# Optimization experiments

Hardware: AMD Instinct MI355X
Metric: run time of the kernel (lower is better)

Reference implementation:

```python
import jax, jax.numpy as jnp
import numpy as np

N = 50000
E = 1600000
EPS = 1e-16


def transformer_conv(x, src, dst, ea, Wq, bq, Wk, bk, Wv, bv, We, Ws, bs):
    # PyG TransformerConv, heads=1, concat=True, root_weight=True
    C = Wq.shape[1]
    q = x @ Wq + bq                      # [N, C]
    k = x @ Wk + bk                      # [N, C]
    v = x @ Wv + bv                      # [N, C]
    e = ea @ We                          # [E, C]
    k_e = k[src] + e                     # per-edge key
    v_e = v[src] + e                     # per-edge value
    score = (q[dst] * k_e).sum(-1) / jnp.sqrt(jnp.asarray(C, x.dtype))  # [E]
    # segment softmax over incoming edges of each dst node
    m = jax.ops.segment_max(score, dst, num_segments=N)
    ex = jnp.exp(score - m[dst])
    denom = jax.ops.segment_sum(ex, dst, num_segments=N)
    alpha = ex / (denom[dst] + EPS)
    out = jax.ops.segment_sum(alpha[:, None] * v_e, dst, num_segments=N)
    return out + x @ Ws + bs             # skip connection


def gcn_conv(x, src, dst, W, b):
    # PyG GCNConv: self-loops + symmetric deg^-1/2 normalization
    n_idx = jnp.arange(N)
    src2 = jnp.concatenate([src, n_idx])
    dst2 = jnp.concatenate([dst, n_idx])
    deg = jax.ops.segment_sum(jnp.ones(E + N, x.dtype), dst2, num_segments=N)
    dinv = jnp.where(deg > 0, jax.lax.rsqrt(deg), 0.0)
    norm = dinv[src2] * dinv[dst2]       # [E+N]
    h = x @ W                            # [N, out]
    out = jax.ops.segment_sum(norm[:, None] * h[src2], dst2, num_segments=N)
    return out + b


def setup_inputs() -> dict:
    key = jax.random.key(0)
    ks = jax.random.split(key, 32)
    d = {}
    d['x'] = jax.random.normal(ks[0], (N, 128), jnp.float32)
    d['edge_index'] = jax.random.randint(ks[1], (2, E), 0, N, jnp.int64)
    d['edge_attr'] = jax.random.normal(ks[2], (E, 16), jnp.float32)
    shapes = dict(
        Wq1=(128, 96), bq1=(96,), Wk1=(128, 96), bk1=(96,), Wv1=(128, 96), bv1=(96,),
        We1=(16, 96), Ws1=(128, 96), bs1=(96,),
        Wq2=(96, 64), bq2=(64,), Wk2=(96, 64), bk2=(64,), Wv2=(96, 64), bv2=(64,),
        We2=(16, 64), Ws2=(96, 64), bs2=(64,),
        Wmu=(64, 32), bmu=(32,), Wls=(64, 32), bls=(32,))
    for i, (name, shp) in enumerate(shapes.items()):
        scale = 1.0 / np.sqrt(shp[0]) if len(shp) == 2 else 0.02
        d[name] = jax.random.normal(ks[3 + i], shp, jnp.float32) * scale
    return d


def reference(x, edge_index, edge_attr,
              Wq1, bq1, Wk1, bk1, Wv1, bv1, We1, Ws1, bs1,
              Wq2, bq2, Wk2, bk2, Wv2, bv2, We2, Ws2, bs2,
              Wmu, bmu, Wls, bls):
    src, dst = edge_index[0], edge_index[1]
    h = jax.nn.relu(transformer_conv(x, src, dst, edge_attr,
                                     Wq1, bq1, Wk1, bk1, Wv1, bv1, We1, Ws1, bs1))
    h = jax.nn.relu(transformer_conv(h, src, dst, edge_attr,
                                     Wq2, bq2, Wk2, bk2, Wv2, bv2, We2, Ws2, bs2))
    mu = gcn_conv(h, src, dst, Wmu, bmu)
    logstd = gcn_conv(h, src, dst, Wls, bls)
    return mu, logstd
```

## Files before the change

kernel.cpp:

```cpp
#include <hip/hip_runtime.h>
#include <math.h>


#define TPB 256
typedef unsigned int uint32;
typedef unsigned short ushort16;
typedef __attribute__((ext_vector_type(4))) float f32x4;
typedef __attribute__((ext_vector_type(8))) short bf16x8;

__device__ __forceinline__ uint32 f2bf(float f) {
    uint32 u = __float_as_uint(f);
    return (u + 0x7fffu + ((u >> 16) & 1u)) >> 16;
}
__device__ __forceinline__ float bf2f(uint32 b) { return __uint_as_float(b << 16); }

__global__ void hist_kernel(const int* __restrict__ dst, int* __restrict__ deg, int E) {
    int i = blockIdx.x * TPB + threadIdx.x;
    if (i < E) atomicAdd(&deg[dst[i]], 1);
}

__global__ __launch_bounds__(1024) void scan1_kernel(const int* __restrict__ deg,
                                                     int* __restrict__ rowp,
                                                     int* __restrict__ bsum, int n) {
    __shared__ int wsum[16];
    __shared__ int woff[16];
    int tid = threadIdx.x;
    int i = blockIdx.x * 1024 + tid;
    int lane = tid & 63, w = tid >> 6;
    int x = (i < n) ? deg[i] : 0;
    int v = x;
#pragma unroll
    for (int off = 1; off < 64; off <<= 1) {
        int t = __shfl_up(v, off, 64);
        if (lane >= off) v += t;
    }
    if (lane == 63) wsum[w] = v;
    __syncthreads();
    if (tid < 64) {
        int s = (tid < 16) ? wsum[tid] : 0;
#pragma unroll
        for (int off = 1; off < 16; off <<= 1) {
            int t = __shfl_up(s, off, 64);
            if (lane >= off) s += t;
        }
        if (tid < 16) woff[tid] = s;
    }
    __syncthreads();
    int incl = v + (w ? woff[w - 1] : 0);
    if (i < n) rowp[i] = incl;
    if (tid == 1023) bsum[blockIdx.x] = incl;
}

__global__ void scan2_kernel(const int* __restrict__ bsum, int* __restrict__ boff, int nb) {
    int tid = threadIdx.x;
    int x = (tid < nb) ? bsum[tid] : 0;
    int v = x;
#pragma unroll
    for (int off = 1; off < 64; off <<= 1) {
        int t = __shfl_up(v, off, 64);
        if (tid >= off) v += t;
    }
    if (tid < nb) boff[tid] = v - x;
}

__global__ __launch_bounds__(1024) void scan3_kernel(const int* __restrict__ deg,
                                                     const int* __restrict__ boff,
                                                     int* __restrict__ rowp,
                                                     int* __restrict__ cursor,
                                                     float* __restrict__ dinv,
                                                     int n, int E) {
    int i = blockIdx.x * 1024 + threadIdx.x;
    if (i < n) {
        int d = deg[i];
        int excl = rowp[i] - d + boff[blockIdx.x];
        rowp[i] = excl;
        cursor[i] = excl;
        dinv[i] = 1.0f / sqrtf((float)(d + 1));
    }
    if (i == 0) rowp[n] = E;
}

__global__ void scatter_kernel(const int* __restrict__ src, const int* __restrict__ dst,
                               const float* __restrict__ EA,
                               int* __restrict__ cursor,
                               int* __restrict__ psrc, ushort16* __restrict__ EAb, int E) {
    int i = blockIdx.x * TPB + threadIdx.x;
    if (i >= E) return;
    int pos = atomicAdd(&cursor[dst[i]], 1);
    psrc[pos] = src[i];
    const float4* e4 = (const float4*)(EA + (size_t)i * 16);
    float4 a = e4[0], b = e4[1], c = e4[2], d = e4[3];
    uint32* o = (uint32*)(EAb + (size_t)pos * 16);
    o[0] = f2bf(a.x) | (f2bf(a.y) << 16);
    o[1] = f2bf(a.z) | (f2bf(a.w) << 16);
    o[2] = f2bf(b.x) | (f2bf(b.y) << 16);
    o[3] = f2bf(b.z) | (f2bf(b.w) << 16);
    o[4] = f2bf(c.x) | (f2bf(c.y) << 16);
    o[5] = f2bf(c.z) | (f2bf(c.w) << 16);
    o[6] = f2bf(d.x) | (f2bf(d.y) << 16);
    o[7] = f2bf(d.z) | (f2bf(d.w) << 16);
}

__global__ void pack_kernel(
    const float* Wq1, const float* Wk1, const float* Wv1, const float* Ws1,
    const float* bq1, const float* bk1, const float* bv1, const float* bs1,
    const float* We1,
    const float* Wq2, const float* Wk2, const float* Wv2, const float* Ws2,
    const float* bq2, const float* bk2, const float* bv2, const float* bs2,
    const float* We2,
    const float* Wmu, const float* bmu, const float* Wls, const float* bls,
    unsigned short* Wc1t, float* bc1, unsigned short* Wc2t, float* bc2,
    float* Wc3, float* bc3) {
    const float s1 = 0.1020620726159658f;
    const float s2 = 0.125f;
    int i = blockIdx.x * TPB + threadIdx.x;
    const int R0 = 448 * 128, R1 = R0 + 320 * 96, R2 = R1 + 64 * 64;
    const int R3 = R2 + 448, R4 = R3 + 320, R5 = R4 + 64;
    if (i < R0) {
        int c = i / 128, kk = i % 128;
        float v = 0.f;
        if (c < 96) v = Wq1[kk * 96 + c] * s1;
        else if (c < 112) {
            int t = c - 96; float a = 0.f;
            for (int u = 0; u < 96; ++u) a += Wq1[kk * 96 + u] * We1[t * 96 + u];
            v = a * s1;
        } else if (c < 304) {
            int tt = c - 112;
            v = (tt & 1) ? Wv1[kk * 96 + (tt >> 1)] : Wk1[kk * 96 + (tt >> 1)];
        } else if (c < 400) v = Ws1[kk * 96 + (c - 304)];
        Wc1t[i] = (unsigned short)f2bf(v);
    } else if (i < R1) {
        int j = i - R0;
        int c = j / 96, kk = j % 96;
        float v = 0.f;
        if (c < 64) v = Wq2[kk * 64 + c] * s2;
        else if (c < 80) {
            int t = c - 64; float a = 0.f;
            for (int u = 0; u < 64; ++u) a += Wq2[kk * 64 + u] * We2[t * 64 + u];
            v = a * s2;
        } else if (c < 208) {
            int tt = c - 80;
            v = (tt & 1) ? Wv2[kk * 64 + (tt >> 1)] : Wk2[kk * 64 + (tt >> 1)];
        } else if (c < 272) v = Ws2[kk * 64 + (c - 208)];
        Wc2t[j] = (unsigned short)f2bf(v);
    } else if (i < R2) {
        int j = i - R1;
        int k = j / 64, c = j % 64;
        Wc3[j] = (c < 32) ? Wmu[k * 32 + c] : Wls[k * 32 + (c - 32)];
    } else if (i < R3) {
        int c = i - R2;
        float v = 0.f;
        if (c < 96) v = bq1[c] * s1;
        else if (c < 112) {
            int t = c - 96; float a = 0.f;
            for (int u = 0; u < 96; ++u) a += bq1[u] * We1[t * 96 + u];
            v = a * s1;
        } else if (c < 304) {
            int tt = c - 112;
            v = (tt & 1) ? bv1[tt >> 1] : bk1[tt >> 1];
        } else if (c < 400) v = bs1[c - 304];
        bc1[c] = v;
    } else if (i < R4) {
        int c = i - R3;
        float v = 0.f;
        if (c < 64) v = bq2[c] * s2;
        else if (c < 80) {
            int t = c - 64; float a = 0.f;
            for (int u = 0; u < 64; ++u) a += bq2[u] * We2[t * 64 + u];
            v = a * s2;
        } else if (c < 208) {
            int tt = c - 80;
            v = (tt & 1) ? bv2[tt >> 1] : bk2[tt >> 1];
        } else if (c < 272) v = bs2[c - 208];
        bc2[c] = v;
    } else if (i < R5) {
        int c = i - R4;
        bc3[c] = (c < 32) ? bmu[c] : bls[c - 32];
    }
}

__global__ void xcvt_kernel(const float* __restrict__ x, unsigned short* __restrict__ xb, int n) {
    int i = blockIdx.x * TPB + threadIdx.x;
    if (i < n) xb[i] = (unsigned short)f2bf(x[i]);
}

__global__ __launch_bounds__(256) void mfma_gemm_kernel(
    const unsigned short* __restrict__ A,
    const unsigned short* __restrict__ Wt,
    const float* __restrict__ bias,
    float* __restrict__ Qs, float* __restrict__ QE,
    uint32* __restrict__ KVp, float* __restrict__ SK,
    int N, int K, int Cq) {
    __shared__ unsigned short As[64][56];
    __shared__ unsigned short Bs[64][56];
    int r0 = blockIdx.x * 64, c0 = blockIdx.y * 64;
    int tid = threadIdx.x;
    int lane = tid & 63, w = tid >> 6;
    int wm = w >> 1, wn = w & 1;
    int l15 = lane & 15, l4 = lane >> 4;
    f32x4 zero = {0.f, 0.f, 0.f, 0.f};
    f32x4 acc[2][2] = {{zero, zero}, {zero, zero}};
    int sr = tid >> 2, sk = (tid & 3) * 8;

    for (int kc = 0; kc < K; kc += 32) {
        bf16x8 av = {};
        int ar = r0 + sr;
        if (ar < N) av = *(const bf16x8*)(A + (size_t)ar * K + kc + sk);
        *(bf16x8*)&As[sr][sk] = av;
        bf16x8 bv = *(const bf16x8*)(Wt + (size_t)(c0 + sr) * K + kc + sk);
        *(bf16x8*)&Bs[sr][sk] = bv;
        __syncthreads();
        bf16x8 af0 = *(const bf16x8*)&As[32 * wm + l15][l4 * 8];
        bf16x8 af1 = *(const bf16x8*)&As[32 * wm + 16 + l15][l4 * 8];
        bf16x8 bf0 = *(const bf16x8*)&Bs[32 * wn + l15][l4 * 8];
        bf16x8 bf1 = *(const bf16x8*)&Bs[32 * wn + 16 + l15][l4 * 8];
        acc[0][0] = __builtin_amdgcn_mfma_f32_16x16x32_bf16(af0, bf0, acc[0][0], 0, 0, 0);
        acc[0][1] = __builtin_amdgcn_mfma_f32_16x16x32_bf16(af0, bf1, acc[0][1], 0, 0, 0);
        acc[1][0] = __builtin_amdgcn_mfma_f32_16x16x32_bf16(af1, bf0, acc[1][0], 0, 0, 0);
        acc[1][1] = __builtin_amdgcn_mfma_f32_16x16x32_bf16(af1, bf1, acc[1][1], 0, 0, 0);
        __syncthreads();
    }

    int qe0 = Cq, kv0 = Cq + 16, sk0 = 3 * Cq + 16, end0 = 4 * Cq + 16;
#pragma unroll
    for (int fm = 0; fm < 2; ++fm) {
#pragma unroll
        for (int fn = 0; fn < 2; ++fn) {
            int cb = c0 + 32 * wn + 16 * fn;
            int c = cb + l15;
            float bia = bias[c];
#pragma unroll
            for (int r = 0; r < 4; ++r) {
                int row = r0 + 32 * wm + 16 * fm + l4 * 4 + r;
                float v = acc[fm][fn][r] + bia;
                float pv = __shfl_xor(v, 1, 64);
                bool ok = row < N;
                if (cb < qe0) {
                    if (ok) Qs[(size_t)row * Cq + c] = v;
                } else if (cb < kv0) {
                    if (ok) QE[(size_t)row * 16 + (c - qe0)] = v;
                } else if (cb < sk0) {
                    if (ok && !(l15 & 1)) {
                        int t = c - kv0;
                        KVp[(size_t)row * Cq + (t >> 1)] = (f2bf(v) << 16) | f2bf(pv);
                    }
                } else if (cb < end0) {
                    if (ok) SK[(size_t)row * Cq + (c - sk0)] = v;
                }
            }
        }
    }
}

template <int C>
__global__ __launch_bounds__(256) void edge_attn_kernel(
    const float* __restrict__ Qs, const float* __restrict__ SK,
    const uint32* __restrict__ KVp,
    const ushort16* __restrict__ EAb, const float* __restrict__ QE,
    const int* __restrict__ rowp, const int* __restrict__ psrc,
    float* __restrict__ Hpre, float* __restrict__ AEA, int N) {
    constexpr int CPL = C / 32;
    int n = blockIdx.x * 4 + (threadIdx.x >> 6);
    if (n >= N) return;
    int lane = threadIdx.x & 63;
    int half = lane >> 5, l = lane & 31, t16 = l & 15;
    bool lo16 = (l < 16);

    float q[CPL], acc[CPL];
#pragma unroll
    for (int j = 0; j < CPL; ++j) { q[j] = Qs[(size_t)n * C + l + 32 * j]; acc[j] = 0.f; }
    float qe = lo16 ? QE[(size_t)n * 16 + t16] : 0.f;
    float d = 0.f, aea = 0.f;
    int eb = rowp[n], ee = rowp[n + 1];

    for (int base = eb + 32 * half; base < ee; base += 64) {
        int cnt = min(32, ee - base);
        int sb = (l < cnt) ? psrc[base + l] : 0;
        for (int i0 = 0; i0 < cnt; i0 += 8) {
            float dots[8], eav[8];
            uint32 kv[8][CPL];
#pragma unroll
            for (int u = 0; u < 8; ++u) {
                int i = i0 + u;
                bool ok = (i < cnt);
                int s = __shfl(sb, i & 31, 32);
                float ea = bf2f(EAb[(size_t)(base + i) * 16 + t16]);
                eav[u] = ok ? ea : 0.f;
                const uint32* kvp = KVp + (size_t)s * C;
                float dt = qe * eav[u];
#pragma unroll
                for (int j = 0; j < CPL; ++j) {
                    uint32 t = kvp[l + 32 * j];
                    kv[u][j] = t;
                    dt = fmaf(q[j], __uint_as_float(t & 0xffff0000u), dt);
                }
                dots[u] = ok ? dt : -1e30f;
            }
#pragma unroll
            for (int a = 0; a < 4; ++a) {
                float x0 = dots[2 * a], x1 = dots[2 * a + 1];
                float z = (lo16 ? x0 : x1) + __shfl_xor(lo16 ? x1 : x0, 16, 64);
                z += __shfl_xor(z, 8, 64);
                z += __shfl_xor(z, 4, 64);
                z += __shfl_xor(z, 2, 64);
                z += __shfl_xor(z, 1, 64);
                float p = __expf(z);
                float p0 = __shfl(p, 0, 32);
                float p1 = __shfl(p, 16, 32);
                d += p0 + p1;
                aea = fmaf(p0, eav[2 * a], fmaf(p1, eav[2 * a + 1], aea));
#pragma unroll
                for (int j = 0; j < CPL; ++j)
                    acc[j] = fmaf(p0, __uint_as_float(kv[2 * a][j] << 16),
                             fmaf(p1, __uint_as_float(kv[2 * a + 1][j] << 16), acc[j]));
            }
        }
    }
    d += __shfl_xor(d, 32, 64);
    aea += __shfl_xor(aea, 32, 64);
    float inv = 1.f / (d + 1e-16f);
#pragma unroll
    for (int j = 0; j < CPL; ++j) {
        float a2 = acc[j] + __shfl_xor(acc[j], 32, 64);
        if (half == 0)
            Hpre[(size_t)n * C + l + 32 * j] = a2 * inv + SK[(size_t)n * C + l + 32 * j];
    }
    if (lane < 16) AEA[(size_t)n * 16 + t16] = aea * inv;
}

template <int C>
__global__ void fixup_relu_kernel(const float* __restrict__ Hpre, const float* __restrict__ AEA,
                                  const float* __restrict__ We,
                                  unsigned short* __restrict__ H1b, int NC) {
    int idx = blockIdx.x * TPB + threadIdx.x;
    if (idx >= NC) return;
    int n = idx / C, c = idx % C;
    const float* a = AEA + (size_t)n * 16;
    float s = Hpre[idx];
#pragma unroll
    for (int t = 0; t < 16; ++t) s += a[t] * We[t * C + c];
    H1b[idx] = (unsigned short)f2bf(fmaxf(s, 0.f));
}

__global__ void fixup2_kernel(const float* __restrict__ Hpre, const float* __restrict__ AEA,
                              const float* __restrict__ We, const float* __restrict__ dinv,
                              uint32* __restrict__ H2p, int N) {
    int idx = blockIdx.x * TPB + threadIdx.x;
    if (idx >= N * 32) return;
    int n = idx >> 5, c = idx & 31;
    const float* a = AEA + (size_t)n * 16;
    float s0 = Hpre[(size_t)n * 64 + c];
    float s1 = Hpre[(size_t)n * 64 + 32 + c];
#pragma unroll
    for (int t = 0; t < 16; ++t) {
        s0 += a[t] * We[t * 64 + c];
        s1 += a[t] * We[t * 64 + 32 + c];
    }
    float dn = dinv[n];
    s0 = fmaxf(s0, 0.f) * dn;
    s1 = fmaxf(s1, 0.f) * dn;
    H2p[idx] = f2bf(s0) | (f2bf(s1) << 16);
}

__global__ __launch_bounds__(256) void gcn_agg_kernel(
    const uint32* __restrict__ H2p, const int* __restrict__ rowp,
    const int* __restrict__ psrc, const float* __restrict__ dinv,
    float* __restrict__ AGG, int N) {
    int n = blockIdx.x * 4 + (threadIdx.x >> 6);
    if (n >= N) return;
    int lane = threadIdx.x & 63, half = lane >> 5, l = lane & 31;
    float s0 = 0.f, s1 = 0.f;
    int eb = rowp[n], ee = rowp[n + 1];
    for (int base = eb + 32 * half; base < ee; base += 64) {
        int cnt = min(32, ee - base);
        int sb = (l < cnt) ? psrc[base + l] : 0;
        for (int i0 = 0; i0 < cnt; i0 += 8) {
            uint32 uu[8];
#pragma unroll
            for (int u = 0; u < 8; ++u) {
                int i = i0 + u;
                int s = __shfl(sb, i & 31, 32);
                uint32 t = H2p[(size_t)s * 32 + l];
                uu[u] = (i < cnt) ? t : 0u;
            }
#pragma unroll
            for (int u = 0; u < 8; ++u) {
                s0 += bf2f(uu[u] & 0xffffu);
                s1 += __uint_as_float(uu[u] & 0xffff0000u);
            }
        }
    }
    s0 += __shfl_xor(s0, 32, 64);
    s1 += __shfl_xor(s1, 32, 64);
    if (half == 0) {
        uint32 u = H2p[(size_t)n * 32 + l];
        float dn = dinv[n];
        AGG[(size_t)n * 64 + l]      = dn * (s0 + bf2f(u & 0xffffu));
        AGG[(size_t)n * 64 + 32 + l] = dn * (s1 + __uint_as_float(u & 0xffff0000u));
    }
}

template <int CT, bool SPLIT>
__global__ __launch_bounds__(256) void gemm_kernel(
    const float* __restrict__ A, const float* __restrict__ W,
    const float* __restrict__ bias, float* __restrict__ Out,
    float* __restrict__ Out2, int N, int K, int C) {
    constexpr int TC = CT / 16;
    __shared__ float As[32][68];
    __shared__ float Bs[32][CT + 4];
    int r0 = blockIdx.x * 64, c0 = blockIdx.y * CT;
    int t = threadIdx.x;
    int tr = t >> 4, tc = t & 15;
    float acc[4][TC];
#pragma unroll
    for (int i = 0; i < 4; ++i)
#pragma unroll
        for (int j = 0; j < TC; ++j) acc[i][j] = 0.f;

    for (int kc = 0; kc < K; kc += 32) {
        int ra = t >> 2, kq = (t & 3) * 8;
        float4 a0 = {0, 0, 0, 0}, a1 = {0, 0, 0, 0};
        int r = r0 + ra;
        if (r < N) {
            const float* ap = A + (size_t)r * K + kc + kq;
            a0 = *(const float4*)ap;
            a1 = *(const float4*)(ap + 4);
        }
        As[kq + 0][ra] = a0.x; As[kq + 1][ra] = a0.y;
        As[kq + 2][ra] = a0.z; As[kq + 3][ra] = a0.w;
        As[kq + 4][ra] = a1.x; As[kq + 5][ra] = a1.y;
        As[kq + 6][ra] = a1.z; As[kq + 7][ra] = a1.w;
        constexpr int PASSES = (32 * CT) / (256 * 8);
#pragma unroll
        for (int p = 0; p < PASSES; ++p) {
            int idx = (t + p * 256) * 8;
            int k = idx / CT, c = idx % CT;
            const float* wp = W + (size_t)(kc + k) * C + c0 + c;
            float4 b0 = *(const float4*)wp;
            float4 b1 = *(const float4*)(wp + 4);
            *(float4*)&Bs[k][c] = b0;
            *(float4*)&Bs[k][c + 4] = b1;
        }
        __syncthreads();
#pragma unroll
        for (int k = 0; k < 32; ++k) {
            float4 av = *(const float4*)&As[k][tr * 4];
            float a[4] = {av.x, av.y, av.z, av.w};
#pragma unroll
            for (int u = 0; u < TC / 4; ++u) {
                float4 bv = *(const float4*)&Bs[k][tc * TC + u * 4];
                float b[4] = {bv.x, bv.y, bv.z, bv.w};
#pragma unroll
                for (int i = 0; i < 4; ++i)
#pragma unroll
                    for (int j = 0; j < 4; ++j) acc[i][u * 4 + j] += a[i] * b[j];
            }
        }
        __syncthreads();
    }
#pragma unroll
    for (int i = 0; i < 4; ++i) {
        int r = r0 + tr * 4 + i;
        if (r >= N) continue;
#pragma unroll
        for (int j = 0; j < TC; ++j) {
            int c = c0 + tc * TC + j;
            float v = acc[i][j] + bias[c];
            if (SPLIT) {
                if (c < 32) Out[(size_t)r * 32 + c] = v;
                else        Out2[(size_t)r * 32 + c - 32] = v;
            } else {
                Out[(size_t)r * C + c] = v;
            }
        }
    }
}

extern "C" void kernel_launch(void* const* d_in, const int* in_sizes, int n_in,
                              void* d_out, int out_size, void* d_ws, size_t ws_size,
                              hipStream_t stream) {
    const float* x   = (const float*)d_in[0];
    const int*   ei  = (const int*)d_in[1];
    const float* ea  = (const float*)d_in[2];
    const float* Wq1 = (const float*)d_in[3];  const float* bq1 = (const float*)d_in[4];
    const float* Wk1 = (const float*)d_in[5];  const float* bk1 = (const float*)d_in[6];
    const float* Wv1 = (const float*)d_in[7];  const float* bv1 = (const float*)d_in[8];
    const float* We1 = (const float*)d_in[9];
    const float* Ws1 = (const float*)d_in[10]; const float* bs1 = (const float*)d_in[11];
    const float* Wq2 = (const float*)d_in[12]; const float* bq2 = (const float*)d_in[13];
    const float* Wk2 = (const float*)d_in[14]; const float* bk2 = (const float*)d_in[15];
    const float* Wv2 = (const float*)d_in[16]; const float* bv2 = (const float*)d_in[17];
    const float* We2 = (const float*)d_in[18];
    const float* Ws2 = (const float*)d_in[19]; const float* bs2 = (const float*)d_in[20];
    const float* Wmu = (const float*)d_in[21]; const float* bmu = (const float*)d_in[22];
    const float* Wls = (const float*)d_in[23]; const float* bls = (const float*)d_in[24];

    int N = in_sizes[0] / 128;
    int E = in_sizes[1] / 2;
    const int* src = ei;
    const int* dst = ei + E;

    char* ws = (char*)d_ws;
    size_t off = 0;
    auto alloc = [&](size_t bytes) -> char* {
        char* p = ws + off;
        off = (off + bytes + 255) & ~(size_t)255;
        return p;
    };
    int*      deg    = (int*)alloc((size_t)N * 4);
    int*      rowp   = (int*)alloc((size_t)(N + 1) * 4);
    int*      cursor = (int*)alloc((size_t)N * 4);
    float*    dinv   = (float*)alloc((size_t)N * 4);
    int*      bsum   = (int*)alloc(256 * 4);
    int*      boff   = (int*)alloc(256 * 4);
    int*      psrc   = (int*)alloc((size_t)E * 4);
    ushort16* EAb    = (ushort16*)alloc((size_t)E * 16 * 2);
    unsigned short* Wc1t = (unsigned short*)alloc(448 * 128 * 2);
    float*    bc1    = (float*)alloc(448 * 4);
    unsigned short* Wc2t = (unsigned short*)alloc(320 * 96 * 2);
    float*    bc2    = (float*)alloc(320 * 4);
    float*    Wc3    = (float*)alloc(64 * 64 * 4);
    float*    bc3    = (float*)alloc(64 * 4);
    unsigned short* xb = (unsigned short*)alloc((size_t)N * 128 * 2);
    float*    Qs   = (float*)alloc((size_t)N * 96 * 4);
    float*    QE   = (float*)alloc((size_t)N * 16 * 4);
    uint32*   KVp  = (uint32*)alloc((size_t)N * 96 * 4);
    float*    SKb  = (float*)alloc((size_t)N * 96 * 4);
    float*    Hpre = (float*)alloc((size_t)N * 96 * 4);
    unsigned short* H1b = (unsigned short*)alloc((size_t)N * 96 * 2);
    float*    AEA  = (float*)alloc((size_t)N * 16 * 4);
    uint32*   H2p  = (uint32*)alloc((size_t)N * 32 * 4);
    float*    AGG  = (float*)alloc((size_t)N * 64 * 4);

    hipMemsetAsync(deg, 0, (size_t)N * 4, stream);
    int ebk = (E + TPB - 1) / TPB;
    int nb1k = (N + 1023) / 1024;
    hist_kernel<<<ebk, TPB, 0, stream>>>(dst, deg, E);
    scan1_kernel<<<nb1k, 1024, 0, stream>>>(deg, rowp, bsum, N);
    scan2_kernel<<<1, 64, 0, stream>>>(bsum, boff, nb1k);
    scan3_kernel<<<nb1k, 1024, 0, stream>>>(deg, boff, rowp, cursor, dinv, N, E);
    scatter_kernel<<<ebk, TPB, 0, stream>>>(src, dst, ea, cursor, psrc, EAb, E);
    pack_kernel<<<364, TPB, 0, stream>>>(Wq1, Wk1, Wv1, Ws1, bq1, bk1, bv1, bs1, We1,
                                         Wq2, Wk2, Wv2, Ws2, bq2, bk2, bv2, bs2, We2,
                                         Wmu, bmu, Wls, bls,
                                         Wc1t, bc1, Wc2t, bc2, Wc3, bc3);
    xcvt_kernel<<<(N * 128 + TPB - 1) / TPB, TPB, 0, stream>>>(x, xb, N * 128);

    int rb = (N + 63) / 64;
    int nb4 = (N + 3) / 4;

    mfma_gemm_kernel<<<dim3(rb, 7), 256, 0, stream>>>(xb, Wc1t, bc1, Qs, QE, KVp, SKb,
                                                      N, 128, 96);
    edge_attn_kernel<96><<<nb4, 256, 0, stream>>>(Qs, SKb, KVp, EAb, QE, rowp, psrc,
                                                  Hpre, AEA, N);
    fixup_relu_kernel<96><<<(N * 96 + TPB - 1) / TPB, TPB, 0, stream>>>(Hpre, AEA, We1,
                                                                        H1b, N * 96);
    mfma_gemm_kernel<<<dim3(rb, 5), 256, 0, stream>>>(H1b, Wc2t, bc2, Qs, QE, KVp, SKb,
                                                      N, 96, 64);
    edge_attn_kernel<64><<<nb4, 256, 0, stream>>>(Qs, SKb, KVp, EAb, QE, rowp, psrc,
                                                  Hpre, AEA, N);
    fixup2_kernel<<<(N * 32 + TPB - 1) / TPB, TPB, 0, stream>>>(Hpre, AEA, We2, dinv, H2p, N);
    gcn_agg_kernel<<<nb4, 256, 0, stream>>>(H2p, rowp, psrc, dinv, AGG, N);
    gemm_kernel<64, true><<<dim3(rb, 1), 256, 0, stream>>>(AGG, Wc3, bc3, (float*)d_out,
                                                           (float*)d_out + (size_t)N * 32,
                                                           N, 64, 64);
}
```

Baseline: 532.6 us.

## Pad CSR rows to multiples of 16 with zero dummy edges to drop bounds checks

Each destination's edge list is rounded up to a multiple of 16, and the extra slots are filled with a dummy source node (index N) whose K/V and H2 rows are zeroed. The attention and GCN aggregation loops then run fixed 8-edge chunks with no shuffle-broadcast of indices and no bounds masks. The attention denominator is corrected by subtracting the pad count, since each pad edge contributes exp(0)=1. The change also folds the x-to-bf16 conversion into pack_kernel, adds nontemporal loads and stores in the edge-ordering kernels, and narrows index maths to 32 bits. The cost is up to 15 wasted edges per node (about 50% more edge traffic at an average degree of 32) and an extra padfill kernel. The unshifted sum exp(z) could also lose precision relative to the correction term.

New measurement: 623.1 us. +17.0%, slower.

```diff
diff --git a/kernel.cpp b/kernel.cpp
--- a/kernel.cpp
+++ b/kernel.cpp
@@ -4,7 +4,7 @@
 
 #define TPB 256
 typedef unsigned int uint32;
-typedef unsigned short ushort16;
+typedef unsigned short u16;
 typedef __attribute__((ext_vector_type(4))) float f32x4;
 typedef __attribute__((ext_vector_type(8))) short bf16x8;
 
@@ -16,18 +16,19 @@
 
 __global__ void hist_kernel(const int* __restrict__ dst, int* __restrict__ deg, int E) {
     int i = blockIdx.x * TPB + threadIdx.x;
-    if (i < E) atomicAdd(&deg[dst[i]], 1);
+    if (i < E) atomicAdd(&deg[__builtin_nontemporal_load(dst + i)], 1);
 }
 
 __global__ __launch_bounds__(1024) void scan1_kernel(const int* __restrict__ deg,
-                                                     int* __restrict__ rowp,
+                                                     int* __restrict__ prowp,
                                                      int* __restrict__ bsum, int n) {
     __shared__ int wsum[16];
     __shared__ int woff[16];
     int tid = threadIdx.x;
     int i = blockIdx.x * 1024 + tid;
     int lane = tid & 63, w = tid >> 6;
-    int x = (i < n) ? deg[i] : 0;
+    int dg = (i < n) ? deg[i] : 0;
+    int x = (dg + 15) & ~15;
     int v = x;
 #pragma unroll
     for (int off = 1; off < 64; off <<= 1) {
@@ -47,11 +48,12 @@
     }
     __syncthreads();
     int incl = v + (w ? woff[w - 1] : 0);
-    if (i < n) rowp[i] = incl;
+    if (i < n) prowp[i] = incl;
     if (tid == 1023) bsum[blockIdx.x] = incl;
 }
 
-__global__ void scan2_kernel(const int* __restrict__ bsum, int* __restrict__ boff, int nb) {
+__global__ void scan2_kernel(const int* __restrict__ bsum, int* __restrict__ boff,
+                             int* __restrict__ prowpN, int nb) {
     int tid = threadIdx.x;
     int x = (tid < nb) ? bsum[tid] : 0;
     int v = x;
@@ -61,44 +63,68 @@
         if (tid >= off) v += t;
     }
     if (tid < nb) boff[tid] = v - x;
+    if (tid == nb - 1) *prowpN = v;
 }
 
 __global__ __launch_bounds__(1024) void scan3_kernel(const int* __restrict__ deg,
                                                      const int* __restrict__ boff,
-                                                     int* __restrict__ rowp,
+                                                     int* __restrict__ prowp,
                                                      int* __restrict__ cursor,
-                                                     float* __restrict__ dinv,
-                                                     int n, int E) {
+                                                     float* __restrict__ dinv, int n) {
     int i = blockIdx.x * 1024 + threadIdx.x;
     if (i < n) {
-        int d = deg[i];
-        int excl = rowp[i] - d + boff[blockIdx.x];
-        rowp[i] = excl;
+        int dg = deg[i];
+        int x = (dg + 15) & ~15;
+        int excl = prowp[i] - x + boff[blockIdx.x];
+        prowp[i] = excl;
         cursor[i] = excl;
-        dinv[i] = 1.0f / sqrtf((float)(d + 1));
-    }
-    if (i == 0) rowp[n] = E;
+        dinv[i] = 1.0f / sqrtf((float)(dg + 1));
+    }
 }
 
 __global__ void scatter_kernel(const int* __restrict__ src, const int* __restrict__ dst,
                                const float* __restrict__ EA,
                                int* __restrict__ cursor,
-                               int* __restrict__ psrc, ushort16* __restrict__ EAb, int E) {
+                               int* __restrict__ psrc, u16* __restrict__ EAb, int E) {
     int i = blockIdx.x * TPB + threadIdx.x;
     if (i >= E) return;
-    int pos = atomicAdd(&cursor[dst[i]], 1);
-    psrc[pos] = src[i];
-    const float4* e4 = (const float4*)(EA + (size_t)i * 16);
-    float4 a = e4[0], b = e4[1], c = e4[2], d = e4[3];
+    int pos = atomicAdd(&cursor[__builtin_nontemporal_load(dst + i)], 1);
+    __builtin_nontemporal_store(__builtin_nontemporal_load(src + i), psrc + pos);
+    const f32x4* e4 = (const f32x4*)(EA + (size_t)i * 16);
+    f32x4 a = __builtin_nontemporal_load(e4);
+    f32x4 b = __builtin_nontemporal_load(e4 + 1);
+    f32x4 c = __builtin_nontemporal_load(e4 + 2);
+    f32x4 d = __builtin_nontemporal_load(e4 + 3);
     uint32* o = (uint32*)(EAb + (size_t)pos * 16);
-    o[0] = f2bf(a.x) | (f2bf(a.y) << 16);
-    o[1] = f2bf(a.z) | (f2bf(a.w) << 16);
-    o[2] = f2bf(b.x) | (f2bf(b.y) << 16);
-    o[3] = f2bf(b.z) | (f2bf(b.w) << 16);
-    o[4] = f2bf(c.x) | (f2bf(c.y) << 16);
-    o[5] = f2bf(c.z) | (f2bf(c.w) << 16);
-    o[6] = f2bf(d.x) | (f2bf(d.y) << 16);
-    o[7] = f2bf(d.z) | (f2bf(d.w) << 16);
+    uint32 w0 = f2bf(a.x) | (f2bf(a.y) << 16);
+    uint32 w1 = f2bf(a.z) | (f2bf(a.w) << 16);
+    uint32 w2 = f2bf(b.x) | (f2bf(b.y) << 16);
+    uint32 w3 = f2bf(b.z) | (f2bf(b.w) << 16);
+    uint32 w4 = f2bf(c.x) | (f2bf(c.y) << 16);
+    uint32 w5 = f2bf(c.z) | (f2bf(c.w) << 16);
+    uint32 w6 = f2bf(d.x) | (f2bf(d.y) << 16);
+    uint32 w7 = f2bf(d.z) | (f2bf(d.w) << 16);
+    __builtin_nontemporal_store(w0, o + 0);
+    __builtin_nontemporal_store(w1, o + 1);
+    __builtin_nontemporal_store(w2, o + 2);
+    __builtin_nontemporal_store(w3, o + 3);
+    __builtin_nontemporal_store(w4, o + 4);
+    __builtin_nontemporal_store(w5, o + 5);
+    __builtin_nontemporal_store(w6, o + 6);
+    __builtin_nontemporal_store(w7, o + 7);
+}
+
+__global__ void padfill_kernel(const int* __restrict__ prowp, const int* __restrict__ deg,
+                               int* __restrict__ psrc, u16* __restrict__ EAb, int N) {
+    int n = blockIdx.x * TPB + threadIdx.x;
+    if (n >= N) return;
+    int p = prowp[n] + deg[n], pe = prowp[n + 1];
+    for (; p < pe; ++p) {
+        psrc[p] = N;
+        uint32* o = (uint32*)(EAb + (size_t)p * 16);
+#pragma unroll
+        for (int j = 0; j < 8; ++j) o[j] = 0u;
+    }
 }
 
 __global__ void pack_kernel(
@@ -109,79 +135,79 @@
     const float* bq2, const float* bk2, const float* bv2, const float* bs2,
     const float* We2,
     const float* Wmu, const float* bmu, const float* Wls, const float* bls,
+    const float* x, unsigned short* xb, int NX,
     unsigned short* Wc1t, float* bc1, unsigned short* Wc2t, float* bc2,
     float* Wc3, float* bc3) {
     const float s1 = 0.1020620726159658f;
     const float s2 = 0.125f;
-    int i = blockIdx.x * TPB + threadIdx.x;
+    int gi = blockIdx.x * TPB + threadIdx.x;
     const int R0 = 448 * 128, R1 = R0 + 320 * 96, R2 = R1 + 64 * 64;
     const int R3 = R2 + 448, R4 = R3 + 320, R5 = R4 + 64;
-    if (i < R0) {
-        int c = i / 128, kk = i % 128;
-        float v = 0.f;
-        if (c < 96) v = Wq1[kk * 96 + c] * s1;
-        else if (c < 112) {
-            int t = c - 96; float a = 0.f;
-            for (int u = 0; u < 96; ++u) a += Wq1[kk * 96 + u] * We1[t * 96 + u];
-            v = a * s1;
-        } else if (c < 304) {
-            int tt = c - 112;
-            v = (tt & 1) ? Wv1[kk * 96 + (tt >> 1)] : Wk1[kk * 96 + (tt >> 1)];
-        } else if (c < 400) v = Ws1[kk * 96 + (c - 304)];
-        Wc1t[i] = (unsigned short)f2bf(v);
-    } else if (i < R1) {
-        int j = i - R0;
-        int c = j / 96, kk = j % 96;
-        float v = 0.f;
-        if (c < 64) v = Wq2[kk * 64 + c] * s2;
-        else if (c < 80) {
-            int t = c - 64; float a = 0.f;
-            for (int u = 0; u < 64; ++u) a += Wq2[kk * 64 + u] * We2[t * 64 + u];
-            v = a * s2;
-        } else if (c < 208) {
-            int tt = c - 80;
-            v = (tt & 1) ? Wv2[kk * 64 + (tt >> 1)] : Wk2[kk * 64 + (tt >> 1)];
-        } else if (c < 272) v = Ws2[kk * 64 + (c - 208)];
-        Wc2t[j] = (unsigned short)f2bf(v);
-    } else if (i < R2) {
-        int j = i - R1;
-        int k = j / 64, c = j % 64;
-        Wc3[j] = (c < 32) ? Wmu[k * 32 + c] : Wls[k * 32 + (c - 32)];
-    } else if (i < R3) {
-        int c = i - R2;
-        float v = 0.f;
-        if (c < 96) v = bq1[c] * s1;
-        else if (c < 112) {
-            int t = c - 96; float a = 0.f;
-            for (int u = 0; u < 96; ++u) a += bq1[u] * We1[t * 96 + u];
-            v = a * s1;
-        } else if (c < 304) {
-            int tt = c - 112;
-            v = (tt & 1) ? bv1[tt >> 1] : bk1[tt >> 1];
-        } else if (c < 400) v = bs1[c - 304];
-        bc1[c] = v;
-    } else if (i < R4) {
-        int c = i - R3;
-        float v = 0.f;
-        if (c < 64) v = bq2[c] * s2;
-        else if (c < 80) {
-            int t = c - 64; float a = 0.f;
-            for (int u = 0; u < 64; ++u) a += bq2[u] * We2[t * 64 + u];
-            v = a * s2;
-        } else if (c < 208) {
-            int tt = c - 80;
-            v = (tt & 1) ? bv2[tt >> 1] : bk2[tt >> 1];
-        } else if (c < 272) v = bs2[c - 208];
-        bc2[c] = v;
-    } else if (i < R5) {
-        int c = i - R4;
-        bc3[c] = (c < 32) ? bmu[c] : bls[c - 32];
-    }
-}
-
-__global__ void xcvt_kernel(const float* __restrict__ x, unsigned short* __restrict__ xb, int n) {
-    int i = blockIdx.x * TPB + threadIdx.x;
-    if (i < n) xb[i] = (unsigned short)f2bf(x[i]);
+    for (int i = gi; i < R5; i += gridDim.x * TPB) {
+        if (i < R0) {
+            int c = i / 128, kk = i % 128;
+            float v = 0.f;
+            if (c < 96) v = Wq1[kk * 96 + c] * s1;
+            else if (c < 112) {
+                int t = c - 96; float a = 0.f;
+                for (int u = 0; u < 96; ++u) a += Wq1[kk * 96 + u] * We1[t * 96 + u];
+                v = a * s1;
+            } else if (c < 304) {
+                int tt = c - 112;
+                v = (tt & 1) ? Wv1[kk * 96 + (tt >> 1)] : Wk1[kk * 96 + (tt >> 1)];
+            } else if (c < 400) v = Ws1[kk * 96 + (c - 304)];
+            Wc1t[i] = (unsigned short)f2bf(v);
+        } else if (i < R1) {
+            int j = i - R0;
+            int c = j / 96, kk = j % 96;
+            float v = 0.f;
+            if (c < 64) v = Wq2[kk * 64 + c] * s2;
+            else if (c < 80) {
+                int t = c - 64; float a = 0.f;
+                for (int u = 0; u < 64; ++u) a += Wq2[kk * 64 + u] * We2[t * 64 + u];
+                v = a * s2;
+            } else if (c < 208) {
+                int tt = c - 80;
+                v = (tt & 1) ? Wv2[kk * 64 + (tt >> 1)] : Wk2[kk * 64 + (tt >> 1)];
+            } else if (c < 272) v = Ws2[kk * 64 + (c - 208)];
+            Wc2t[j] = (unsigned short)f2bf(v);
+        } else if (i < R2) {
+            int j = i - R1;
+            int k = j / 64, c = j % 64;
+            Wc3[j] = (c < 32) ? Wmu[k * 32 + c] : Wls[k * 32 + (c - 32)];
+        } else if (i < R3) {
+            int c = i - R2;
+            float v = 0.f;
+            if (c < 96) v = bq1[c] * s1;
+            else if (c < 112) {
+                int t = c - 96; float a = 0.f;
+                for (int u = 0; u < 96; ++u) a += bq1[u] * We1[t * 96 + u];
+                v = a * s1;
+            } else if (c < 304) {
+                int tt = c - 112;
+                v = (tt & 1) ? bv1[tt >> 1] : bk1[tt >> 1];
+            } else if (c < 400) v = bs1[c - 304];
+            bc1[c] = v;
+        } else if (i < R4) {
+            int c = i - R3;
+            float v = 0.f;
+            if (c < 64) v = bq2[c] * s2;
+            else if (c < 80) {
+                int t = c - 64; float a = 0.f;
+                for (int u = 0; u < 64; ++u) a += bq2[u] * We2[t * 64 + u];
+                v = a * s2;
+            } else if (c < 208) {
+                int tt = c - 80;
+                v = (tt & 1) ? bv2[tt >> 1] : bk2[tt >> 1];
+            } else if (c < 272) v = bs2[c - 208];
+            bc2[c] = v;
+        } else {
+            int c = i - R4;
+            bc3[c] = (c < 32) ? bmu[c] : bls[c - 32];
+        }
+    }
+    for (int i = gi; i < NX; i += gridDim.x * TPB)
+        xb[i] = (unsigned short)f2bf(x[i]);
 }
 
 __global__ __launch_bounds__(256) void mfma_gemm_kernel(
@@ -256,8 +282,9 @@
 __global__ __launch_bounds__(256) void edge_attn_kernel(
     const float* __restrict__ Qs, const float* __restrict__ SK,
     const uint32* __restrict__ KVp,
-    const ushort16* __restrict__ EAb, const float* __restrict__ QE,
-    const int* __restrict__ rowp, const int* __restrict__ psrc,
+    const u16* __restrict__ EAb, const float* __restrict__ QE,
+    const int* __restrict__ prowp, const int* __restrict__ deg,
+    const int* __restrict__ psrc,
     float* __restrict__ Hpre, float* __restrict__ AEA, int N) {
     constexpr int CPL = C / 32;
     int n = blockIdx.x * 4 + (threadIdx.x >> 6);
@@ -266,66 +293,63 @@
     int half = lane >> 5, l = lane & 31, t16 = l & 15;
     bool lo16 = (l < 16);
 
+    uint32 nC = (uint32)n * C;
     float q[CPL], acc[CPL];
 #pragma unroll
-    for (int j = 0; j < CPL; ++j) { q[j] = Qs[(size_t)n * C + l + 32 * j]; acc[j] = 0.f; }
-    float qe = lo16 ? QE[(size_t)n * 16 + t16] : 0.f;
+    for (int j = 0; j < CPL; ++j) { q[j] = Qs[nC + l + 32 * j]; acc[j] = 0.f; }
+    float qe = lo16 ? QE[(uint32)n * 16 + t16] : 0.f;
     float d = 0.f, aea = 0.f;
-    int eb = rowp[n], ee = rowp[n + 1];
-
-    for (int base = eb + 32 * half; base < ee; base += 64) {
-        int cnt = min(32, ee - base);
-        int sb = (l < cnt) ? psrc[base + l] : 0;
-        for (int i0 = 0; i0 < cnt; i0 += 8) {
-            float dots[8], eav[8];
-            uint32 kv[8][CPL];
-#pragma unroll
-            for (int u = 0; u < 8; ++u) {
-                int i = i0 + u;
-                bool ok = (i < cnt);
-                int s = __shfl(sb, i & 31, 32);
-                float ea = bf2f(EAb[(size_t)(base + i) * 16 + t16]);
-                eav[u] = ok ? ea : 0.f;
-                const uint32* kvp = KVp + (size_t)s * C;
-                float dt = qe * eav[u];
-#pragma unroll
-                for (int j = 0; j < CPL; ++j) {
-                    uint32 t = kvp[l + 32 * j];
-                    kv[u][j] = t;
-                    dt = fmaf(q[j], __uint_as_float(t & 0xffff0000u), dt);
-                }
-                dots[u] = ok ? dt : -1e30f;
+    int eb = prowp[n], ee = prowp[n + 1];
+
+    for (int base = eb + 8 * half; base < ee; base += 16) {
+        const int* sp = psrc + base;
+        const u16* ep = EAb + (size_t)base * 16 + t16;
+        float dots[8], eav[8];
+        uint32 kv[8][CPL];
+#pragma unroll
+        for (int u = 0; u < 8; ++u) {
+            int s = __builtin_nontemporal_load(sp + u);
+            eav[u] = bf2f(__builtin_nontemporal_load(ep + u * 16));
+            uint32 off = (uint32)s * C + l;
+            float dt = qe * eav[u];
+#pragma unroll
+            for (int j = 0; j < CPL; ++j) {
+                uint32 t = KVp[off + 32 * j];
+                kv[u][j] = t;
+                dt = fmaf(q[j], __uint_as_float(t & 0xffff0000u), dt);
             }
-#pragma unroll
-            for (int a = 0; a < 4; ++a) {
-                float x0 = dots[2 * a], x1 = dots[2 * a + 1];
-                float z = (lo16 ? x0 : x1) + __shfl_xor(lo16 ? x1 : x0, 16, 64);
-                z += __shfl_xor(z, 8, 64);
-                z += __shfl_xor(z, 4, 64);
-                z += __shfl_xor(z, 2, 64);
-                z += __shfl_xor(z, 1, 64);
-                float p = __expf(z);
-                float p0 = __shfl(p, 0, 32);
-                float p1 = __shfl(p, 16, 32);
-                d += p0 + p1;
-                aea = fmaf(p0, eav[2 * a], fmaf(p1, eav[2 * a + 1], aea));
-#pragma unroll
-                for (int j = 0; j < CPL; ++j)
-                    acc[j] = fmaf(p0, __uint_as_float(kv[2 * a][j] << 16),
-                             fmaf(p1, __uint_as_float(kv[2 * a + 1][j] << 16), acc[j]));
-            }
+            dots[u] = dt;
+        }
+#pragma unroll
+        for (int a = 0; a < 4; ++a) {
+            float x0 = dots[2 * a], x1 = dots[2 * a + 1];
+            float z = (lo16 ? x0 : x1) + __shfl_xor(lo16 ? x1 : x0, 16, 64);
+            z += __shfl_xor(z, 8, 64);
+            z += __shfl_xor(z, 4, 64);
+            z += __shfl_xor(z, 2, 64);
+            z += __shfl_xor(z, 1, 64);
+            float p = __expf(z);
+            float p0 = __shfl(p, 0, 32);
+            float p1 = __shfl(p, 16, 32);
+            d += p0 + p1;
+            aea = fmaf(p0, eav[2 * a], fmaf(p1, eav[2 * a + 1], aea));
+#pragma unroll
+            for (int j = 0; j < CPL; ++j)
+                acc[j] = fmaf(p0, __uint_as_float(kv[2 * a][j] << 16),
+                         fmaf(p1, __uint_as_float(kv[2 * a + 1][j] << 16), acc[j]));
         }
     }
     d += __shfl_xor(d, 32, 64);
     aea += __shfl_xor(aea, 32, 64);
+    d -= (float)((ee - eb) - deg[n]);
     float inv = 1.f / (d + 1e-16f);
 #pragma unroll
     for (int j = 0; j < CPL; ++j) {
         float a2 = acc[j] + __shfl_xor(acc[j], 32, 64);
         if (half == 0)
-            Hpre[(size_t)n * C + l + 32 * j] = a2 * inv + SK[(size_t)n * C + l + 32 * j];
-    }
-    if (lane < 16) AEA[(size_t)n * 16 + t16] = aea * inv;
+            Hpre[nC + l + 32 * j] = a2 * inv + SK[nC + l + 32 * j];
+    }
+    if (lane < 16) AEA[(uint32)n * 16 + t16] = aea * inv;
 }
 
 template <int C>
@@ -363,40 +387,31 @@
 }
 
 __global__ __launch_bounds__(256) void gcn_agg_kernel(
-    const uint32* __restrict__ H2p, const int* __restrict__ rowp,
+    const uint32* __restrict__ H2p, const int* __restrict__ prowp,
     const int* __restrict__ psrc, const float* __restrict__ dinv,
     float* __restrict__ AGG, int N) {
     int n = blockIdx.x * 4 + (threadIdx.x >> 6);
     if (n >= N) return;
     int lane = threadIdx.x & 63, half = lane >> 5, l = lane & 31;
     float s0 = 0.f, s1 = 0.f;
-    int eb = rowp[n], ee = rowp[n + 1];
-    for (int base = eb + 32 * half; base < ee; base += 64) {
-        int cnt = min(32, ee - base);
-        int sb = (l < cnt) ? psrc[base + l] : 0;
-        for (int i0 = 0; i0 < cnt; i0 += 8) {
-            uint32 uu[8];
-#pragma unroll
-            for (int u = 0; u < 8; ++u) {
-                int i = i0 + u;
-                int s = __shfl(sb, i & 31, 32);
-                uint32 t = H2p[(size_t)s * 32 + l];
-                uu[u] = (i < cnt) ? t : 0u;
-            }
-#pragma unroll
-            for (int u = 0; u < 8; ++u) {
-                s0 += bf2f(uu[u] & 0xffffu);
-                s1 += __uint_as_float(uu[u] & 0xffff0000u);
-            }
+    int eb = prowp[n], ee = prowp[n + 1];
+    for (int base = eb + 8 * half; base < ee; base += 16) {
+        const int* sp = psrc + base;
+#pragma unroll
+        for (int u = 0; u < 8; ++u) {
+            int s = __builtin_nontemporal_load(sp + u);
+            uint32 t = H2p[(uint32)s * 32 + l];
+            s0 += bf2f(t & 0xffffu);
+            s1 += __uint_as_float(t & 0xffff0000u);
         }
     }
     s0 += __shfl_xor(s0, 32, 64);
     s1 += __shfl_xor(s1, 32, 64);
     if (half == 0) {
-        uint32 u = H2p[(size_t)n * 32 + l];
+        uint32 u = H2p[(uint32)n * 32 + l];
         float dn = dinv[n];
-        AGG[(size_t)n * 64 + l]      = dn * (s0 + bf2f(u & 0xffffu));
-        AGG[(size_t)n * 64 + 32 + l] = dn * (s1 + __uint_as_float(u & 0xffff0000u));
+        AGG[(uint32)n * 64 + l]      = dn * (s0 + bf2f(u & 0xffffu));
+        AGG[(uint32)n * 64 + 32 + l] = dn * (s1 + __uint_as_float(u & 0xffff0000u));
     }
 }
 
@@ -499,6 +514,7 @@
     int E = in_sizes[1] / 2;
     const int* src = ei;
     const int* dst = ei + E;
+    int E2max = E + 16 * N;
 
     char* ws = (char*)d_ws;
     size_t off = 0;
@@ -508,13 +524,13 @@
         return p;
     };
     int*      deg    = (int*)alloc((size_t)N * 4);
-    int*      rowp   = (int*)alloc((size_t)(N + 1) * 4);
+    int*      prowp  = (int*)alloc((size_t)(N + 1) * 4);
     int*      cursor = (int*)alloc((size_t)N * 4);
     float*    dinv   = (float*)alloc((size_t)N * 4);
     int*      bsum   = (int*)alloc(256 * 4);
     int*      boff   = (int*)alloc(256 * 4);
-    int*      psrc   = (int*)alloc((size_t)E * 4);
-    ushort16* EAb    = (ushort16*)alloc((size_t)E * 16 * 2);
+    int*      psrc   = (int*)alloc((size_t)E2max * 4);
+    u16*      EAb    = (u16*)alloc((size_t)E2max * 16 * 2);
     unsigned short* Wc1t = (unsigned short*)alloc(448 * 128 * 2);
     float*    bc1    = (float*)alloc(448 * 4);
     unsigned short* Wc2t = (unsigned short*)alloc(320 * 96 * 2);
@@ -524,43 +540,48 @@
     unsigned short* xb = (unsigned short*)alloc((size_t)N * 128 * 2);
     float*    Qs   = (float*)alloc((size_t)N * 96 * 4);
     float*    QE   = (float*)alloc((size_t)N * 16 * 4);
-    uint32*   KVp  = (uint32*)alloc((size_t)N * 96 * 4);
+    uint32*   KVp  = (uint32*)alloc((size_t)(N + 1) * 96 * 4);
     float*    SKb  = (float*)alloc((size_t)N * 96 * 4);
     float*    Hpre = (float*)alloc((size_t)N * 96 * 4);
     unsigned short* H1b = (unsigned short*)alloc((size_t)N * 96 * 2);
     float*    AEA  = (float*)alloc((size_t)N * 16 * 4);
-    uint32*   H2p  = (uint32*)alloc((size_t)N * 32 * 4);
+    uint32*   H2p  = (uint32*)alloc((size_t)(N + 1) * 32 * 4);
     float*    AGG  = (float*)alloc((size_t)N * 64 * 4);
 
-    hipMemsetAsync(deg, 0, (size_t)N * 4, stream);
+    (void)hipMemsetAsync(deg, 0, (size_t)N * 4, stream);
+    (void)hipMemsetAsync(KVp + (size_t)N * 96, 0, 96 * 4, stream);
+    (void)hipMemsetAsync(H2p + (size_t)N * 32, 0, 32 * 4, stream);
+
     int ebk = (E + TPB - 1) / TPB;
     int nb1k = (N + 1023) / 1024;
+    int nbN = (N + TPB - 1) / TPB;
     hist_kernel<<<ebk, TPB, 0, stream>>>(dst, deg, E);
-    scan1_kernel<<<nb1k, 1024, 0, stream>>>(deg, rowp, bsum, N);
-    scan2_kernel<<<1, 64, 0, stream>>>(bsum, boff, nb1k);
-    scan3_kernel<<<nb1k, 1024, 0, stream>>>(deg, boff, rowp, cursor, dinv, N, E);
+    scan1_kernel<<<nb1k, 1024, 0, stream>>>(deg, prowp, bsum, N);
+    scan2_kernel<<<1, 64, 0, stream>>>(bsum, boff, prowp + N, nb1k);
+    scan3_kernel<<<nb1k, 1024, 0, stream>>>(deg, boff, prowp, cursor, dinv, N);
     scatter_kernel<<<ebk, TPB, 0, stream>>>(src, dst, ea, cursor, psrc, EAb, E);
+    padfill_kernel<<<nbN, TPB, 0, stream>>>(prowp, deg, psrc, EAb, N);
     pack_kernel<<<364, TPB, 0, stream>>>(Wq1, Wk1, Wv1, Ws1, bq1, bk1, bv1, bs1, We1,
                                          Wq2, Wk2, Wv2, Ws2, bq2, bk2, bv2, bs2, We2,
-                                         Wmu, bmu, Wls, bls,
+                                         Wmu, bmu, Wls, bls, x, xb, N * 128,
                                          Wc1t, bc1, Wc2t, bc2, Wc3, bc3);
-    xcvt_kernel<<<(N * 128 + TPB - 1) / TPB, TPB, 0, stream>>>(x, xb, N * 128);
 
     int rb = (N + 63) / 64;
     int nb4 = (N + 3) / 4;
 
     mfma_gemm_kernel<<<dim3(rb, 7), 256, 0, stream>>>(xb, Wc1t, bc1, Qs, QE, KVp, SKb,
                                                       N, 128, 96);
-    edge_attn_kernel<96><<<nb4, 256, 0, stream>>>(Qs, SKb, KVp, EAb, QE, rowp, psrc,
+    edge_attn_kernel<96><<<nb4, 256, 0, stream>>>(Qs, SKb, KVp, EAb, QE, prowp, deg, psrc,
                                                   Hpre, AEA, N);
     fixup_relu_kernel<96><<<(N * 96 + TPB - 1) / TPB, TPB, 0, stream>>>(Hpre, AEA, We1,
                                                                         H1b, N * 96);
     mfma_gemm_kernel<<<dim3(rb, 5), 256, 0, stream>>>(H1b, Wc2t, bc2, Qs, QE, KVp, SKb,
                                                       N, 96, 64);
-    edge_attn_kernel<64><<<nb4, 256, 0, stream>>>(Qs, SKb, KVp, EAb, QE, rowp, psrc,
+    (void)hipMemsetAsync(KVp + (size_t)N * 64, 0, 64 * 4, stream);
+    edge_attn_kernel<64><<<nb4, 256, 0, stream>>>(Qs, SKb, KVp, EAb, QE, prowp, deg, psrc,
                                                   Hpre, AEA, N);
     fixup2_kernel<<<(N * 32 + TPB - 1) / TPB, TPB, 0, stream>>>(Hpre, AEA, We2, dinv, H2p, N);
-    gcn_agg_kernel<<<nb4, 256, 0, stream>>>(H2p, rowp, psrc, dinv, AGG, N);
+    gcn_agg_kernel<<<nb4, 256, 0, stream>>>(H2p, prowp, psrc, dinv, AGG, N);
     gemm_kernel<64, true><<<dim3(rb, 1), 256, 0, stream>>>(AGG, Wc3, bc3, (float*)d_out,
                                                            (float*)d_out + (size_t)N * 32,
                                                            N, 64, 64);
```
